# Performance work log

Measured on AMD Instinct MI355X. Metric: run time of the kernel, lower is better.

## Reference

```python
import jax, jax.numpy as jnp
import numpy as np

B, D_IN, D_OUT = 16384, 512, 64
H1, H2, GH = 64, 32, 32
E_SH, G, E_G = 2, 2, 2
LN_EPS = 1e-5


def _expert(v, w1, b1, w2, b2, w3, b3, gamma, beta):
    # MLP(input->64->32->D_OUT, Swish on hiddens, linear final) + LayerNorm(D_OUT)
    h = jax.nn.silu(v @ w1 + b1)
    h = jax.nn.silu(h @ w2 + b2)
    o = h @ w3 + b3
    mu = jnp.mean(o, axis=-1, keepdims=True)
    var = jnp.mean((o - mu) ** 2, axis=-1, keepdims=True)
    return gamma * (o - mu) * jax.lax.rsqrt(var + LN_EPS) + beta


def _gate(v, w1, b1, w2, b2):
    # MLP(input->32->E, Swish hidden, linear final) then softmax over experts
    h = jax.nn.silu(v @ w1 + b1)
    return jax.nn.softmax(h @ w2 + b2, axis=-1)


def setup_inputs() -> dict:
    key = jax.random.key(0)
    ks = iter(jax.random.split(key, 16))

    def rn(shape, scale=0.02):
        return jax.random.normal(next(ks), shape, dtype=jnp.float32) * scale

    return {
        "v": jax.random.normal(next(ks), (B, D_IN), dtype=jnp.float32),
        # shared experts (stacked over expert axis E_SH)
        "sw1": rn((E_SH, D_IN, H1)), "sb1": jnp.zeros((E_SH, H1), jnp.float32),
        "sw2": rn((E_SH, H1, H2)), "sb2": jnp.zeros((E_SH, H2), jnp.float32),
        "sw3": rn((E_SH, H2, D_OUT)), "sb3": jnp.zeros((E_SH, D_OUT), jnp.float32),
        "sgam": jnp.ones((E_SH, D_OUT), jnp.float32), "sbet": jnp.zeros((E_SH, D_OUT), jnp.float32),
        # shared gate
        "sgw1": rn((D_IN, GH)), "sgb1": jnp.zeros((GH,), jnp.float32),
        "sgw2": rn((GH, E_SH)), "sgb2": jnp.zeros((E_SH,), jnp.float32),
        # group experts (stacked over [G, E_G])
        "gw1": rn((G, E_G, D_IN, H1)), "gb1": jnp.zeros((G, E_G, H1), jnp.float32),
        "gw2": rn((G, E_G, H1, H2)), "gb2": jnp.zeros((G, E_G, H2), jnp.float32),
        "gw3": rn((G, E_G, H2, D_OUT)), "gb3": jnp.zeros((G, E_G, D_OUT), jnp.float32),
        "ggam": jnp.ones((G, E_G, D_OUT), jnp.float32), "gbet": jnp.zeros((G, E_G, D_OUT), jnp.float32),
        # group gates (stacked over G)
        "ggw1": rn((G, D_IN, GH)), "ggb1": jnp.zeros((G, GH), jnp.float32),
        "ggw2": rn((G, GH, E_G)), "ggb2": jnp.zeros((G, E_G), jnp.float32),
    }


def reference(v, sw1, sb1, sw2, sb2, sw3, sb3, sgam, sbet,
              sgw1, sgb1, sgw2, sgb2,
              gw1, gb1, gw2, gb2, gw3, gb3, ggam, gbet,
              ggw1, ggb1, ggw2, ggb2):
    expert_v = jax.vmap(_expert, in_axes=(None, 0, 0, 0, 0, 0, 0, 0, 0))
    # shared branch
    sh_outs = expert_v(v, sw1, sb1, sw2, sb2, sw3, sb3, sgam, sbet)   # [E, B, D]
    sh_w = _gate(v, sgw1, sgb1, sgw2, sgb2)                           # [B, E]
    z_shared = jnp.einsum('ebd,be->bd', sh_outs, sh_w)                # [B, D]
    # group branches (vmap over group axis G, inner vmap over experts)
    grp_expert = jax.vmap(expert_v, in_axes=(None, 0, 0, 0, 0, 0, 0, 0, 0))
    g_outs = grp_expert(v, gw1, gb1, gw2, gb2, gw3, gb3, ggam, gbet)  # [G, E, B, D]
    g_w = jax.vmap(_gate, in_axes=(None, 0, 0, 0, 0))(v, ggw1, ggb1, ggw2, ggb2)  # [G, B, E]
    z_groups = jnp.einsum('gebd,gbe->gbd', g_outs, g_w)               # [G, B, D]
    # stack (group_0, group_1, shared) -> [G+1, B, D]
    return jnp.concatenate([z_groups, z_shared[None]], axis=0)
```

## Files before the change

### kernel.cpp

```cpp
#include <hip/hip_runtime.h>

typedef short short8 __attribute__((ext_vector_type(8)));
typedef float f32x4 __attribute__((ext_vector_type(4)));

enum : unsigned {
  OFF_B1  = 0u,
  OFF_B2  = 491520u,
  OFF_B3  = 516096u,
  OFF_b1  = 540672u,
  OFF_b2  = 542592u,
  OFF_b3  = 543360u,
  OFF_gam = 544896u,
  OFF_bet = 546432u,
  OFF_gw2 = 547968u,
  OFF_gb2 = 548736u
};

__device__ __forceinline__ unsigned short f2bf(float x) {
  unsigned u = __builtin_bit_cast(unsigned, x);
  return (unsigned short)((u + 0x7fffu + ((u >> 16) & 1u)) >> 16);
}
__device__ __forceinline__ float bf2f(unsigned short b) {
  unsigned u = ((unsigned)b) << 16;
  return __builtin_bit_cast(float, u);
}
__device__ __forceinline__ float silu(float x) { return x / (1.f + __expf(-x)); }
__device__ __forceinline__ int fragk(int lane, int j) {
  return ((lane >> 4) << 2) + (j & 3) + ((j >> 2) << 4);
}

__global__ void pack_W(
    const float* __restrict__ sw1, const float* __restrict__ sb1,
    const float* __restrict__ sw2, const float* __restrict__ sb2,
    const float* __restrict__ sw3, const float* __restrict__ sb3,
    const float* __restrict__ sgam, const float* __restrict__ sbet,
    const float* __restrict__ sgw1, const float* __restrict__ sgb1,
    const float* __restrict__ sgw2, const float* __restrict__ sgb2,
    const float* __restrict__ gw1, const float* __restrict__ gb1,
    const float* __restrict__ gw2, const float* __restrict__ gb2,
    const float* __restrict__ gw3, const float* __restrict__ gb3,
    const float* __restrict__ ggam, const float* __restrict__ gbet,
    const float* __restrict__ ggw1, const float* __restrict__ ggb1,
    const float* __restrict__ ggw2, const float* __restrict__ ggb2,
    unsigned char* __restrict__ ws) {
  int id = blockIdx.x * blockDim.x + threadIdx.x;

  if (id < 30720) {
    int lane = id & 63; int rest = id >> 6;
    int nt = rest % 10; int rk = rest / 10;
    int ks = rk & 15; int branch = rk >> 4;
    int col = nt * 16 + (lane & 15);
    short8 o;
#pragma unroll
    for (int j = 0; j < 8; ++j) {
      int k = ks * 32 + fragk(lane, j);
      float w;
      if (branch < 2) {
        if (col < 128) w = gw1[((branch * 2 + (col >> 6)) * 512 + k) * 64 + (col & 63)];
        else           w = ggw1[(branch * 512 + k) * 32 + (col - 128)];
      } else {
        if (col < 128) w = sw1[((col >> 6) * 512 + k) * 64 + (col & 63)];
        else           w = sgw1[k * 32 + (col - 128)];
      }
      o[j] = (short)f2bf(w);
    }
    ((short8*)(ws + OFF_B1))[id] = o;
    return;
  }
  id -= 30720;
  if (id < 1536) {
    int lane = id & 63; int rest = id >> 6;
    int nt = rest & 1, kk = (rest >> 1) & 1, eid = rest >> 2;
    int n = nt * 16 + (lane & 15);
    short8 o;
#pragma unroll
    for (int j = 0; j < 8; ++j) {
      int k = kk * 32 + fragk(lane, j);
      float w = (eid < 4) ? gw2[(eid * 64 + k) * 32 + n] : sw2[((eid - 4) * 64 + k) * 32 + n];
      o[j] = (short)f2bf(w);
    }
    ((short8*)(ws + OFF_B2))[id] = o;
    return;
  }
  id -= 1536;
  if (id < 1536) {
    int lane = id & 63; int rest = id >> 6;
    int nt = rest & 3, eid = rest >> 2;
    int n = nt * 16 + (lane & 15);
    short8 o;
#pragma unroll
    for (int j = 0; j < 8; ++j) {
      int k = fragk(lane, j);
      float w = (eid < 4) ? gw3[(eid * 32 + k) * 64 + n] : sw3[((eid - 4) * 32 + k) * 64 + n];
      o[j] = (short)f2bf(w);
    }
    ((short8*)(ws + OFF_B3))[id] = o;
    return;
  }
  id -= 1536;
  if (id < 480) {
    int branch = id / 160, col = id % 160;
    float w;
    if (col < 128) w = (branch < 2) ? gb1[(branch * 2 + (col >> 6)) * 64 + (col & 63)]
                                    : sb1[(col >> 6) * 64 + (col & 63)];
    else           w = (branch < 2) ? ggb1[branch * 32 + (col - 128)] : sgb1[col - 128];
    ((float*)(ws + OFF_b1))[id] = w;
    return;
  }
  id -= 480;
  if (id < 192) { ((float*)(ws + OFF_b2))[id] = (id < 128) ? gb2[id] : sb2[id - 128]; return; }
  id -= 192;
  if (id < 384) { ((float*)(ws + OFF_b3))[id] = (id < 256) ? gb3[id] : sb3[id - 256]; return; }
  id -= 384;
  if (id < 384) { ((float*)(ws + OFF_gam))[id] = (id < 256) ? ggam[id] : sgam[id - 256]; return; }
  id -= 384;
  if (id < 384) { ((float*)(ws + OFF_bet))[id] = (id < 256) ? gbet[id] : sbet[id - 256]; return; }
  id -= 384;
  if (id < 192) { int branch = id / 64; ((float*)(ws + OFF_gw2))[id] = (branch < 2) ? ggw2[id] : sgw2[id % 64]; return; }
  id -= 192;
  if (id < 6)  { ((float*)(ws + OFF_gb2))[id] = (id < 4) ? ggb2[id] : sgb2[id % 2]; return; }
}

__global__ __launch_bounds__(256) void fused_main(const float* __restrict__ v,
                                                  const unsigned char* __restrict__ ws,
                                                  float* __restrict__ out) {
  const int tid  = threadIdx.x;
  const int lane = tid & 63, wave = tid >> 6;
  const int branch = blockIdx.y;
  const int mtile = blockIdx.x * 4 + wave;
  const int col16 = lane & 15, g4 = lane >> 4;

  const short8* B1 = (const short8*)(ws + OFF_B1) + branch * 16 * 640;
  const short8* B2 = (const short8*)(ws + OFF_B2);
  const short8* B3 = (const short8*)(ws + OFF_B3);
  const float* b1c  = (const float*)(ws + OFF_b1) + branch * 160;
  const float* b2c  = (const float*)(ws + OFF_b2);
  const float* b3c  = (const float*)(ws + OFF_b3);
  const float* gamc = (const float*)(ws + OFF_gam);
  const float* betc = (const float*)(ws + OFF_bet);
  const float* gw2c = (const float*)(ws + OFF_gw2) + branch * 64;
  const float* gb2c = (const float*)(ws + OFF_gb2) + branch * 2;

  __shared__ short8 b1s[2][640];
  __shared__ unsigned short h1l[4][16][164];
  __shared__ unsigned short h2l[4][16][68];
  __shared__ float gatew[4][16][2];

  {
    short8 r0 = B1[tid];
    short8 r1 = B1[tid + 256];
    b1s[0][tid] = r0;
    b1s[0][tid + 256] = r1;
    if (tid < 128) b1s[0][tid + 512] = B1[tid + 512];
  }

  f32x4 acc[10];
#pragma unroll
  for (int nt = 0; nt < 10; ++nt) acc[nt] = (f32x4){0.f, 0.f, 0.f, 0.f};

  const float* vrow = v + (mtile * 16 + col16) * 512 + (g4 << 2);

  for (int ks = 0; ks < 16; ++ks) {
    const int cur = ks & 1;
    short8 s0, s1, s2;
    if (ks < 15) {
      const short8* src = B1 + (ks + 1) * 640;
      s0 = src[tid];
      s1 = src[tid + 256];
      if (tid < 128) s2 = src[tid + 512];
    }
    __syncthreads();
    float4 lo = *(const float4*)(vrow + ks * 32);
    float4 hi = *(const float4*)(vrow + ks * 32 + 16);
    short8 a;
    a[0] = (short)f2bf(lo.x); a[1] = (short)f2bf(lo.y);
    a[2] = (short)f2bf(lo.z); a[3] = (short)f2bf(lo.w);
    a[4] = (short)f2bf(hi.x); a[5] = (short)f2bf(hi.y);
    a[6] = (short)f2bf(hi.z); a[7] = (short)f2bf(hi.w);
#pragma unroll
    for (int nt = 0; nt < 10; ++nt) {
      short8 b = b1s[cur][nt * 64 + lane];
      acc[nt] = __builtin_amdgcn_mfma_f32_16x16x32_bf16(a, b, acc[nt], 0, 0, 0);
    }
    if (ks < 15) {
      const int nxt = cur ^ 1;
      b1s[nxt][tid] = s0;
      b1s[nxt][tid + 256] = s1;
      if (tid < 128) b1s[nxt][tid + 512] = s2;
    }
  }

#pragma unroll
  for (int nt = 0; nt < 10; ++nt) {
    int col = nt * 16 + col16;
    float bb = b1c[col];
#pragma unroll
    for (int r = 0; r < 4; ++r) {
      int row = (g4 << 2) + r;
      h1l[wave][row][col] = f2bf(silu(acc[nt][r] + bb));
    }
  }
  __syncthreads();

  {
    int rowg = (lane >> 1) & 15;
    int e = lane & 1;
    float logit = gb2c[e];
#pragma unroll 8
    for (int j = 0; j < 32; ++j)
      logit += bf2f(h1l[wave][rowg][128 + j]) * gw2c[j * 2 + e];
    float other = __shfl_xor(logit, 1, 64);
    float mx = fmaxf(logit, other);
    float a0 = __expf(logit - mx), a1 = __expf(other - mx);
    if (lane < 32) gatew[wave][rowg][e] = a0 / (a0 + a1);
  }

#pragma unroll
  for (int e2 = 0; e2 < 2; ++e2) {
    const int eid = (branch < 2) ? branch * 2 + e2 : 4 + e2;
    f32x4 a2[2];
    a2[0] = (f32x4){0.f, 0.f, 0.f, 0.f};
    a2[1] = (f32x4){0.f, 0.f, 0.f, 0.f};
#pragma unroll
    for (int kk = 0; kk < 2; ++kk) {
      const unsigned short* p = &h1l[wave][col16][e2 * 64 + kk * 32 + (g4 << 2)];
      union { short8 s; unsigned u[4]; } af;
      af.u[0] = *(const unsigned*)p;        af.u[1] = *(const unsigned*)(p + 2);
      af.u[2] = *(const unsigned*)(p + 16); af.u[3] = *(const unsigned*)(p + 18);
#pragma unroll
      for (int nt = 0; nt < 2; ++nt) {
        short8 b = B2[((eid * 2 + kk) * 2 + nt) * 64 + lane];
        a2[nt] = __builtin_amdgcn_mfma_f32_16x16x32_bf16(af.s, b, a2[nt], 0, 0, 0);
      }
    }
#pragma unroll
    for (int nt = 0; nt < 2; ++nt) {
      int c2 = nt * 16 + col16;
      float bb = b2c[eid * 32 + c2];
#pragma unroll
      for (int r = 0; r < 4; ++r) {
        int row = (g4 << 2) + r;
        h2l[wave][row][e2 * 32 + c2] = f2bf(silu(a2[nt][r] + bb));
      }
    }
  }
  __syncthreads();

  float z[4][4];
#pragma unroll
  for (int r = 0; r < 4; ++r)
#pragma unroll
    for (int nt = 0; nt < 4; ++nt) z[r][nt] = 0.f;

#pragma unroll
  for (int e2 = 0; e2 < 2; ++e2) {
    const int eid = (branch < 2) ? branch * 2 + e2 : 4 + e2;
    f32x4 a3[4];
#pragma unroll
    for (int nt = 0; nt < 4; ++nt) a3[nt] = (f32x4){0.f, 0.f, 0.f, 0.f};
    const unsigned short* p = &h2l[wave][col16][e2 * 32 + (g4 << 2)];
    union { short8 s; unsigned u[4]; } af;
    af.u[0] = *(const unsigned*)p;        af.u[1] = *(const unsigned*)(p + 2);
    af.u[2] = *(const unsigned*)(p + 16); af.u[3] = *(const unsigned*)(p + 18);
#pragma unroll
    for (int nt = 0; nt < 4; ++nt) {
      short8 b = B3[(eid * 4 + nt) * 64 + lane];
      a3[nt] = __builtin_amdgcn_mfma_f32_16x16x32_bf16(af.s, b, a3[nt], 0, 0, 0);
    }
#pragma unroll
    for (int r = 0; r < 4; ++r) {
      float o[4], s = 0.f, s2 = 0.f;
#pragma unroll
      for (int nt = 0; nt < 4; ++nt) {
        o[nt] = a3[nt][r] + b3c[eid * 64 + nt * 16 + col16];
        s += o[nt]; s2 += o[nt] * o[nt];
      }
#pragma unroll
      for (int m = 1; m < 16; m <<= 1) {
        s  += __shfl_xor(s, m, 64);
        s2 += __shfl_xor(s2, m, 64);
      }
      float mu  = s * 0.015625f;
      float var = s2 * 0.015625f - mu * mu;
      float inv = rsqrtf(var + 1e-5f);
      int row = (g4 << 2) + r;
      float wt = gatew[wave][row][e2];
#pragma unroll
      for (int nt = 0; nt < 4; ++nt) {
        int c = nt * 16 + col16;
        float ln = (o[nt] - mu) * inv * gamc[eid * 64 + c] + betc[eid * 64 + c];
        z[r][nt] += wt * ln;
      }
    }
  }

#pragma unroll
  for (int r = 0; r < 4; ++r) {
    int grow = mtile * 16 + (g4 << 2) + r;
#pragma unroll
    for (int nt = 0; nt < 4; ++nt)
      out[(branch * 16384 + grow) * 64 + nt * 16 + col16] = z[r][nt];
  }
}

extern "C" void kernel_launch(void* const* d_in, const int* in_sizes, int n_in,
                              void* d_out, int out_size, void* d_ws, size_t ws_size,
                              hipStream_t stream) {
  const float* v    = (const float*)d_in[0];
  const float* sw1  = (const float*)d_in[1];
  const float* sb1  = (const float*)d_in[2];
  const float* sw2  = (const float*)d_in[3];
  const float* sb2  = (const float*)d_in[4];
  const float* sw3  = (const float*)d_in[5];
  const float* sb3  = (const float*)d_in[6];
  const float* sgam = (const float*)d_in[7];
  const float* sbet = (const float*)d_in[8];
  const float* sgw1 = (const float*)d_in[9];
  const float* sgb1 = (const float*)d_in[10];
  const float* sgw2 = (const float*)d_in[11];
  const float* sgb2 = (const float*)d_in[12];
  const float* gw1  = (const float*)d_in[13];
  const float* gb1  = (const float*)d_in[14];
  const float* gw2  = (const float*)d_in[15];
  const float* gb2  = (const float*)d_in[16];
  const float* gw3  = (const float*)d_in[17];
  const float* gb3  = (const float*)d_in[18];
  const float* ggam = (const float*)d_in[19];
  const float* gbet = (const float*)d_in[20];
  const float* ggw1 = (const float*)d_in[21];
  const float* ggb1 = (const float*)d_in[22];
  const float* ggw2 = (const float*)d_in[23];
  const float* ggb2 = (const float*)d_in[24];
  unsigned char* ws = (unsigned char*)d_ws;
  float* out = (float*)d_out;

  pack_W<<<dim3(140), dim3(256), 0, stream>>>(
      sw1, sb1, sw2, sb2, sw3, sb3, sgam, sbet, sgw1, sgb1, sgw2, sgb2,
      gw1, gb1, gw2, gb2, gw3, gb3, ggam, gbet, ggw1, ggb1, ggw2, ggb2, ws);
  fused_main<<<dim3(256, 3), dim3(256), 0, stream>>>(v, ws, out);
}
```

Baseline: 143.6 us.

## Keep MLP hidden activations in registers via transposed MFMA, remap block order

Swaps MFMA operand order so each lane holds the output transposed (one row, consecutive columns). The layer-1 and layer-2 results can then be packed straight into bf16 A-fragments for the next MFMA, with no trip through shared memory. This removes the h1/h2/gate LDS buffers and two block-wide barriers, vectorises the bias, gamma, beta and output accesses, and simplifies the gate and LayerNorm reductions to two cross-lane shuffles. It also flattens the grid and swizzles block indices so the three branches for the same rows run close together, and adds a min-blocks launch bound. The risks are higher register pressure and possible spills under the occupancy hint.

```diff
diff --git a/kernel.cpp b/kernel.cpp
--- a/kernel.cpp
+++ b/kernel.cpp
@@ -20,13 +20,15 @@
   unsigned u = __builtin_bit_cast(unsigned, x);
   return (unsigned short)((u + 0x7fffu + ((u >> 16) & 1u)) >> 16);
 }
-__device__ __forceinline__ float bf2f(unsigned short b) {
-  unsigned u = ((unsigned)b) << 16;
-  return __builtin_bit_cast(float, u);
-}
 __device__ __forceinline__ float silu(float x) { return x / (1.f + __expf(-x)); }
 __device__ __forceinline__ int fragk(int lane, int j) {
   return ((lane >> 4) << 2) + (j & 3) + ((j >> 2) << 4);
+}
+__device__ __forceinline__ short8 pack8(const f32x4& a, const f32x4& b) {
+  short8 o;
+#pragma unroll
+  for (int i = 0; i < 4; ++i) { o[i] = (short)f2bf(a[i]); o[4 + i] = (short)f2bf(b[i]); }
+  return o;
 }
 
 __global__ void pack_W(
@@ -121,13 +123,14 @@
   if (id < 6)  { ((float*)(ws + OFF_gb2))[id] = (id < 4) ? ggb2[id] : sgb2[id % 2]; return; }
 }
 
-__global__ __launch_bounds__(256) void fused_main(const float* __restrict__ v,
-                                                  const unsigned char* __restrict__ ws,
-                                                  float* __restrict__ out) {
+__global__ __launch_bounds__(256, 4) void fused_main(const float* __restrict__ v,
+                                                     const unsigned char* __restrict__ ws,
+                                                     float* __restrict__ out) {
   const int tid  = threadIdx.x;
   const int lane = tid & 63, wave = tid >> 6;
-  const int branch = blockIdx.y;
-  const int mtile = blockIdx.x * 4 + wave;
+  const int wrk = (blockIdx.x & 7) * 96 + (blockIdx.x >> 3);
+  const int branch = wrk % 3;
+  const int mtile = (wrk / 3) * 4 + wave;
   const int col16 = lane & 15, g4 = lane >> 4;
 
   const short8* B1 = (const short8*)(ws + OFF_B1) + branch * 16 * 640;
@@ -142,9 +145,6 @@
   const float* gb2c = (const float*)(ws + OFF_gb2) + branch * 2;
 
   __shared__ short8 b1s[2][640];
-  __shared__ unsigned short h1l[4][16][164];
-  __shared__ unsigned short h2l[4][16][68];
-  __shared__ float gatew[4][16][2];
 
   {
     short8 r0 = B1[tid];
@@ -180,7 +180,7 @@
 #pragma unroll
     for (int nt = 0; nt < 10; ++nt) {
       short8 b = b1s[cur][nt * 64 + lane];
-      acc[nt] = __builtin_amdgcn_mfma_f32_16x16x32_bf16(a, b, acc[nt], 0, 0, 0);
+      acc[nt] = __builtin_amdgcn_mfma_f32_16x16x32_bf16(b, a, acc[nt], 0, 0, 0);
     }
     if (ks < 15) {
       const int nxt = cur ^ 1;
@@ -190,30 +190,40 @@
     }
   }
 
+  f32x4 h[10];
 #pragma unroll
   for (int nt = 0; nt < 10; ++nt) {
-    int col = nt * 16 + col16;
-    float bb = b1c[col];
+    f32x4 bb = *(const f32x4*)(b1c + nt * 16 + (g4 << 2));
+#pragma unroll
+    for (int r = 0; r < 4; ++r) h[nt][r] = silu(acc[nt][r] + bb[r]);
+  }
+
+  float w0, w1;
+  {
+    float p0 = 0.f, p1 = 0.f;
 #pragma unroll
     for (int r = 0; r < 4; ++r) {
-      int row = (g4 << 2) + r;
-      h1l[wave][row][col] = f2bf(silu(acc[nt][r] + bb));
-    }
-  }
-  __syncthreads();
-
-  {
-    int rowg = (lane >> 1) & 15;
-    int e = lane & 1;
-    float logit = gb2c[e];
-#pragma unroll 8
-    for (int j = 0; j < 32; ++j)
-      logit += bf2f(h1l[wave][rowg][128 + j]) * gw2c[j * 2 + e];
-    float other = __shfl_xor(logit, 1, 64);
-    float mx = fmaxf(logit, other);
-    float a0 = __expf(logit - mx), a1 = __expf(other - mx);
-    if (lane < 32) gatew[wave][rowg][e] = a0 / (a0 + a1);
-  }
+      float2 wa = *(const float2*)(gw2c + ((g4 << 2) + r) * 2);
+      float2 wb = *(const float2*)(gw2c + (16 + (g4 << 2) + r) * 2);
+      p0 += h[8][r] * wa.x + h[9][r] * wb.x;
+      p1 += h[8][r] * wa.y + h[9][r] * wb.y;
+    }
+    p0 += __shfl_xor(p0, 16, 64); p0 += __shfl_xor(p0, 32, 64);
+    p1 += __shfl_xor(p1, 16, 64); p1 += __shfl_xor(p1, 32, 64);
+    float l0 = p0 + gb2c[0], l1 = p1 + gb2c[1];
+    float mx = fmaxf(l0, l1);
+    float e0 = __expf(l0 - mx), e1 = __expf(l1 - mx);
+    float inv = 1.f / (e0 + e1);
+    w0 = e0 * inv; w1 = e1 * inv;
+  }
+
+  short8 h1f[4];
+#pragma unroll
+  for (int f = 0; f < 4; ++f) h1f[f] = pack8(h[2 * f], h[2 * f + 1]);
+
+  f32x4 z[4];
+#pragma unroll
+  for (int nt = 0; nt < 4; ++nt) z[nt] = (f32x4){0.f, 0.f, 0.f, 0.f};
 
 #pragma unroll
   for (int e2 = 0; e2 < 2; ++e2) {
@@ -223,84 +233,63 @@
     a2[1] = (f32x4){0.f, 0.f, 0.f, 0.f};
 #pragma unroll
     for (int kk = 0; kk < 2; ++kk) {
-      const unsigned short* p = &h1l[wave][col16][e2 * 64 + kk * 32 + (g4 << 2)];
-      union { short8 s; unsigned u[4]; } af;
-      af.u[0] = *(const unsigned*)p;        af.u[1] = *(const unsigned*)(p + 2);
-      af.u[2] = *(const unsigned*)(p + 16); af.u[3] = *(const unsigned*)(p + 18);
+      short8 hf = h1f[e2 * 2 + kk];
 #pragma unroll
       for (int nt = 0; nt < 2; ++nt) {
         short8 b = B2[((eid * 2 + kk) * 2 + nt) * 64 + lane];
-        a2[nt] = __builtin_amdgcn_mfma_f32_16x16x32_bf16(af.s, b, a2[nt], 0, 0, 0);
+        a2[nt] = __builtin_amdgcn_mfma_f32_16x16x32_bf16(b, hf, a2[nt], 0, 0, 0);
       }
     }
-#pragma unroll
-    for (int nt = 0; nt < 2; ++nt) {
-      int c2 = nt * 16 + col16;
-      float bb = b2c[eid * 32 + c2];
+    f32x4 h2a, h2b;
+    {
+      f32x4 ba = *(const f32x4*)(b2c + eid * 32 + (g4 << 2));
+      f32x4 bb = *(const f32x4*)(b2c + eid * 32 + 16 + (g4 << 2));
 #pragma unroll
       for (int r = 0; r < 4; ++r) {
-        int row = (g4 << 2) + r;
-        h2l[wave][row][e2 * 32 + c2] = f2bf(silu(a2[nt][r] + bb));
+        h2a[r] = silu(a2[0][r] + ba[r]);
+        h2b[r] = silu(a2[1][r] + bb[r]);
       }
     }
-  }
-  __syncthreads();
-
-  float z[4][4];
-#pragma unroll
-  for (int r = 0; r < 4; ++r)
-#pragma unroll
-    for (int nt = 0; nt < 4; ++nt) z[r][nt] = 0.f;
-
-#pragma unroll
-  for (int e2 = 0; e2 < 2; ++e2) {
-    const int eid = (branch < 2) ? branch * 2 + e2 : 4 + e2;
+    short8 h2f = pack8(h2a, h2b);
+
     f32x4 a3[4];
 #pragma unroll
     for (int nt = 0; nt < 4; ++nt) a3[nt] = (f32x4){0.f, 0.f, 0.f, 0.f};
-    const unsigned short* p = &h2l[wave][col16][e2 * 32 + (g4 << 2)];
-    union { short8 s; unsigned u[4]; } af;
-    af.u[0] = *(const unsigned*)p;        af.u[1] = *(const unsigned*)(p + 2);
-    af.u[2] = *(const unsigned*)(p + 16); af.u[3] = *(const unsigned*)(p + 18);
 #pragma unroll
     for (int nt = 0; nt < 4; ++nt) {
       short8 b = B3[(eid * 4 + nt) * 64 + lane];
-      a3[nt] = __builtin_amdgcn_mfma_f32_16x16x32_bf16(af.s, b, a3[nt], 0, 0, 0);
-    }
-#pragma unroll
-    for (int r = 0; r < 4; ++r) {
-      float o[4], s = 0.f, s2 = 0.f;
-#pragma unroll
-      for (int nt = 0; nt < 4; ++nt) {
-        o[nt] = a3[nt][r] + b3c[eid * 64 + nt * 16 + col16];
-        s += o[nt]; s2 += o[nt] * o[nt];
+      a3[nt] = __builtin_amdgcn_mfma_f32_16x16x32_bf16(b, h2f, a3[nt], 0, 0, 0);
+    }
+    float o[4][4], s = 0.f, s2 = 0.f;
+#pragma unroll
+    for (int nt = 0; nt < 4; ++nt) {
+      f32x4 bb = *(const f32x4*)(b3c + eid * 64 + nt * 16 + (g4 << 2));
+#pragma unroll
+      for (int r = 0; r < 4; ++r) {
+        o[nt][r] = a3[nt][r] + bb[r];
+        s += o[nt][r]; s2 += o[nt][r] * o[nt][r];
       }
-#pragma unroll
-      for (int m = 1; m < 16; m <<= 1) {
-        s  += __shfl_xor(s, m, 64);
-        s2 += __shfl_xor(s2, m, 64);
-      }
-      float mu  = s * 0.015625f;
-      float var = s2 * 0.015625f - mu * mu;
-      float inv = rsqrtf(var + 1e-5f);
-      int row = (g4 << 2) + r;
-      float wt = gatew[wave][row][e2];
-#pragma unroll
-      for (int nt = 0; nt < 4; ++nt) {
-        int c = nt * 16 + col16;
-        float ln = (o[nt] - mu) * inv * gamc[eid * 64 + c] + betc[eid * 64 + c];
-        z[r][nt] += wt * ln;
-      }
-    }
-  }
-
-#pragma unroll
-  for (int r = 0; r < 4; ++r) {
-    int grow = mtile * 16 + (g4 << 2) + r;
-#pragma unroll
-    for (int nt = 0; nt < 4; ++nt)
-      out[(branch * 16384 + grow) * 64 + nt * 16 + col16] = z[r][nt];
-  }
+    }
+    s  += __shfl_xor(s, 16, 64);  s  += __shfl_xor(s, 32, 64);
+    s2 += __shfl_xor(s2, 16, 64); s2 += __shfl_xor(s2, 32, 64);
+    float mu  = s * 0.015625f;
+    float var = s2 * 0.015625f - mu * mu;
+    float inv = rsqrtf(var + 1e-5f);
+    float wt = (e2 == 0) ? w0 : w1;
+#pragma unroll
+    for (int nt = 0; nt < 4; ++nt) {
+      f32x4 gm = *(const f32x4*)(gamc + eid * 64 + nt * 16 + (g4 << 2));
+      f32x4 bt = *(const f32x4*)(betc + eid * 64 + nt * 16 + (g4 << 2));
+#pragma unroll
+      for (int r = 0; r < 4; ++r)
+        z[nt][r] += wt * ((o[nt][r] - mu) * inv * gm[r] + bt[r]);
+    }
+  }
+
+  float* orow = out + (branch * 16384 + mtile * 16 + col16) * 64 + (g4 << 2);
+#pragma unroll
+  for (int nt = 0; nt < 4; ++nt)
+    *(f32x4*)(orow + nt * 16) = z[nt];
 }
 
 extern "C" void kernel_launch(void* const* d_in, const int* in_sizes, int n_in,
@@ -337,5 +326,5 @@
   pack_W<<<dim3(140), dim3(256), 0, stream>>>(
       sw1, sb1, sw2, sb2, sw3, sb3, sgam, sbet, sgw1, sgb1, sgw2, sgb2,
       gw1, gb1, gw2, gb2, gw3, gb3, ggam, gbet, ggw1, ggb1, ggw2, ggb2, ws);
-  fused_main<<<dim3(256, 3), dim3(256), 0, stream>>>(v, ws, out);
-}
+  fused_main<<<dim3(768), dim3(256), 0, stream>>>(v, ws, out);
+}
```

Result: no change. 144.9 us (+0.9%).
